# Optimization experiments

Measured on AMD Instinct MI355X. Metric: run time of the kernel, lower is better.

## Reference

```python
import jax, jax.numpy as jnp
import numpy as np

H = 16
D_MODEL = 1024
D_K = D_MODEL // H
B, S = 8, 1024


def setup_inputs() -> dict:
    key = jax.random.key(0)
    ks = jax.random.split(key, 11)
    scale = 1.0 / np.sqrt(D_MODEL)
    inp = {
        "query": jax.random.normal(ks[0], (B, S, D_MODEL), jnp.float32),
        "key_": jax.random.normal(ks[1], (B, S, D_MODEL), jnp.float32),
        "value": jax.random.normal(ks[2], (B, S, D_MODEL), jnp.float32),
        "w_q": jax.random.normal(ks[3], (D_MODEL, D_MODEL), jnp.float32) * scale,
        "b_q": jnp.zeros((D_MODEL,), jnp.float32),
        "w_k": jax.random.normal(ks[4], (D_MODEL, D_MODEL), jnp.float32) * scale,
        "b_k": jnp.zeros((D_MODEL,), jnp.float32),
        "w_v": jax.random.normal(ks[5], (D_MODEL, D_MODEL), jnp.float32) * scale,
        "b_v": jnp.zeros((D_MODEL,), jnp.float32),
        "w_o": jax.random.normal(ks[6], (D_MODEL, D_MODEL), jnp.float32) * scale,
        "b_o": jnp.zeros((D_MODEL,), jnp.float32),
    }
    return inp


def reference(query, key_, value, w_q, b_q, w_k, b_k, w_v, b_v, w_o, b_o):
    # Linear projections (torch Linear: x @ W.T + b), then split heads: [B,S,D] -> [B,H,S,d_k]
    def proj(x, w, b):
        y = jnp.einsum("bsd,ed->bse", x, w) + b
        return y.reshape(B, S, H, D_K).transpose(0, 2, 1, 3)

    q = proj(query, w_q, b_q)
    k = proj(key_, w_k, b_k)
    v = proj(value, w_v, b_v)

    # Scaled dot-product attention (mask=None, dropout p=0 -> identity)
    scores = jnp.einsum("bhqd,bhkd->bhqk", q, k) / jnp.sqrt(jnp.float32(D_K))
    attn = jax.nn.softmax(scores, axis=-1)
    ctx = jnp.einsum("bhqk,bhkd->bhqd", attn, v)  # [B,H,S,d_k]

    # Merge heads and final output projection
    ctx = ctx.transpose(0, 2, 1, 3).reshape(B, S, D_MODEL)
    return jnp.einsum("bsd,ed->bse", ctx, w_o) + b_o
```

## Files before the change

kernel.cpp:

```cpp
#include <hip/hip_runtime.h>
#include <hip/hip_bf16.h>

#define NH 16
#define DK 64
#define BB 8
#define SS 1024
#define DM 1024
#define MTOT (BB * SS)

typedef float f4v __attribute__((ext_vector_type(4)));
typedef short s16v8 __attribute__((ext_vector_type(8)));
typedef unsigned short u16v4 __attribute__((ext_vector_type(4)));
typedef unsigned short u16v8 __attribute__((ext_vector_type(8)));

__device__ __forceinline__ unsigned short f2bf(float x) {
    unsigned int u = __float_as_uint(x);
    u += 0x7FFFu + ((u >> 16) & 1u);
    return (unsigned short)(u >> 16);
}

__device__ __forceinline__ void gload16(const void* g, void* l) {
    __builtin_amdgcn_global_load_lds(
        (const __attribute__((address_space(1))) void*)g,
        (__attribute__((address_space(3))) void*)l, 16, 0, 0);
}

struct Src7 { const float* p[7]; };

__global__ __launch_bounds__(256) void cvt_all(Src7 sp, unsigned short* __restrict__ dst) {
    const size_t e = ((size_t)blockIdx.x * 256 + threadIdx.x) * 8;
    const int unit = (int)(e >> 20);
    int t; size_t base;
    if (unit < 8)       { t = 0; base = 0; }
    else if (unit < 16) { t = 1; base = (size_t)8 << 20; }
    else if (unit < 24) { t = 2; base = (size_t)16 << 20; }
    else                { t = 3 + (unit - 24); base = (size_t)unit << 20; }
    const float* s = sp.p[t] + (e - base);
    f4v a = *(const f4v*)s;
    f4v b = *(const f4v*)(s + 4);
    u16v8 o;
    o[0] = f2bf(a[0]); o[1] = f2bf(a[1]); o[2] = f2bf(a[2]); o[3] = f2bf(a[3]);
    o[4] = f2bf(b[0]); o[5] = f2bf(b[1]); o[6] = f2bf(b[2]); o[7] = f2bf(b[3]);
    *(u16v8*)(dst + e) = o;
}

template <int MODE>
__global__ __launch_bounds__(256) void gemm_bf16(const unsigned short* __restrict__ X,
                                                 const unsigned short* __restrict__ W,
                                                 const float* __restrict__ bias,
                                                 void* __restrict__ Yv) {
    __shared__ unsigned short As[128 * 32];
    __shared__ unsigned short Bs[128 * 32];
    const int tid = threadIdx.x;
    const int wv = tid >> 6, l = tid & 63;
    const int lq = l & 15, g = l >> 4;
    const int wr = wv >> 1, wc = wv & 1;
    const int m0 = blockIdx.y * 128, n0 = blockIdx.x * 128;

    f4v acc[4][4];
#pragma unroll
    for (int i = 0; i < 4; ++i)
#pragma unroll
        for (int j = 0; j < 4; ++j) acc[i][j] = (f4v){0.f, 0.f, 0.f, 0.f};

    for (int kt = 0; kt < DM / 32; ++kt) {
        const int k0 = kt * 32;
        __syncthreads();
#pragma unroll
        for (int p = 0; p < 2; ++p) {
            const int u = p * 256 + tid;
            const int row = u >> 2, kc = u & 3;
            gload16(X + (size_t)(m0 + row) * DM + k0 + kc * 8, As + (size_t)u * 8);
            gload16(W + (size_t)(n0 + row) * DM + k0 + kc * 8, Bs + (size_t)u * 8);
        }
        __syncthreads();

        s16v8 a[4], b[4];
#pragma unroll
        for (int i = 0; i < 4; ++i)
            a[i] = *(const s16v8*)(As + (wr * 64 + i * 16 + lq) * 32 + g * 8);
#pragma unroll
        for (int j = 0; j < 4; ++j)
            b[j] = *(const s16v8*)(Bs + (wc * 64 + j * 16 + lq) * 32 + g * 8);
#pragma unroll
        for (int i = 0; i < 4; ++i)
#pragma unroll
            for (int j = 0; j < 4; ++j)
                acc[i][j] = __builtin_amdgcn_mfma_f32_16x16x32_bf16(a[i], b[j], acc[i][j], 0, 0, 0);
    }

#pragma unroll
    for (int j = 0; j < 4; ++j) {
        const int col = n0 + wc * 64 + j * 16 + lq;
        const float bv = bias[col];
#pragma unroll
        for (int i = 0; i < 4; ++i) {
#pragma unroll
            for (int r = 0; r < 4; ++r) {
                const int row = m0 + wr * 64 + i * 16 + g * 4 + r;
                const float val = acc[i][j][r] + bv;
                if (MODE == 0) {
                    ((float*)Yv)[(size_t)row * DM + col] = val;
                } else {
                    const int b_ = row >> 10, s_ = row & (SS - 1);
                    const int h_ = col >> 6, d_ = col & (DK - 1);
                    ((unsigned short*)Yv)[((size_t)(b_ * NH + h_) * SS + s_) * DK + d_] = f2bf(val);
                }
            }
        }
    }
}

__global__ __launch_bounds__(256) void transpose_v(const unsigned short* __restrict__ Vp,
                                                   unsigned short* __restrict__ VpT) {
    __shared__ unsigned short Ts[64][68];
    const int bx = blockIdx.x;
    const int bh = bx >> 4, kt = bx & 15;
    const unsigned short* src = Vp + (size_t)bh * (SS * DK) + (size_t)kt * 64 * DK;
    unsigned short* dst = VpT + (size_t)bh * (SS * DK) + kt * 64;
    const int t = threadIdx.x;
#pragma unroll
    for (int p = 0; p < 4; ++p) {
        const int idx = p * 1024 + t * 4;
        const int key = idx >> 6, d = idx & 63;
        *(u16v4*)&Ts[key][d] = *(const u16v4*)(src + (size_t)key * DK + d);
    }
    __syncthreads();
#pragma unroll
    for (int p = 0; p < 4; ++p) {
        const int idx = p * 1024 + t * 4;
        const int d = idx >> 6, k4 = idx & 63;
        u16v4 o;
        o[0] = Ts[k4 + 0][d]; o[1] = Ts[k4 + 1][d];
        o[2] = Ts[k4 + 2][d]; o[3] = Ts[k4 + 3][d];
        *(u16v4*)(dst + (size_t)d * SS + k4) = o;
    }
}

__global__ __launch_bounds__(256) void attn_mfma(const unsigned short* __restrict__ Qp,
                                                 const unsigned short* __restrict__ Kp,
                                                 const unsigned short* __restrict__ Vt,
                                                 unsigned short* __restrict__ ctx) {
    __shared__ unsigned short Ks[4096];
    __shared__ unsigned short Vs[4096];
    __shared__ unsigned short Ps[4][16 * 72];
    const int tid = threadIdx.x;
    const int wv = tid >> 6, l = tid & 63;
    const int lq = l & 15, g = l >> 4;
    const int bh = blockIdx.x, q0 = blockIdx.y * 64;

    const unsigned short* Qb = Qp + ((size_t)bh * SS + q0 + wv * 16) * DK;
    const unsigned short* Kb = Kp + (size_t)bh * SS * DK;
    const unsigned short* Vb = Vt + (size_t)bh * DK * SS;

    s16v8 qf[2];
    qf[0] = *(const s16v8*)(Qb + lq * DK + g * 8);
    qf[1] = *(const s16v8*)(Qb + lq * DK + 32 + g * 8);

    f4v O[4];
#pragma unroll
    for (int od = 0; od < 4; ++od) O[od] = (f4v){0.f, 0.f, 0.f, 0.f};
    float m_r[4] = {-1e30f, -1e30f, -1e30f, -1e30f};
    float l_r[4] = {0.f, 0.f, 0.f, 0.f};

    for (int t = 0; t < SS / 64; ++t) {
        __syncthreads();
#pragma unroll
        for (int p = 0; p < 2; ++p) {
            const int u = p * 256 + tid;
            gload16(Kb + (size_t)(t * 64 + (u & 63)) * DK + (u >> 6) * 8, Ks + (size_t)u * 8);
            gload16(Vb + (size_t)(u & 63) * SS + t * 64 + (u >> 6) * 8, Vs + (size_t)u * 8);
        }
        __syncthreads();

        f4v s[4];
#pragma unroll
        for (int ct = 0; ct < 4; ++ct) s[ct] = (f4v){0.f, 0.f, 0.f, 0.f};
#pragma unroll
        for (int kk = 0; kk < 2; ++kk) {
#pragma unroll
            for (int ct = 0; ct < 4; ++ct) {
                s16v8 kf = *(const s16v8*)(Ks + ((kk * 4 + g) * 64 + ct * 16 + lq) * 8);
                s[ct] = __builtin_amdgcn_mfma_f32_16x16x32_bf16(qf[kk], kf, s[ct], 0, 0, 0);
            }
        }

        float rs[4], corr[4];
#pragma unroll
        for (int r = 0; r < 4; ++r) {
            float v = fmaxf(fmaxf(s[0][r], s[1][r]), fmaxf(s[2][r], s[3][r])) * 0.125f;
            v = fmaxf(v, __shfl_xor(v, 1));
            v = fmaxf(v, __shfl_xor(v, 2));
            v = fmaxf(v, __shfl_xor(v, 4));
            v = fmaxf(v, __shfl_xor(v, 8));
            const float mn = fmaxf(m_r[r], v);
            corr[r] = __expf(m_r[r] - mn);
            m_r[r] = mn;
            rs[r] = 0.f;
        }
#pragma unroll
        for (int ct = 0; ct < 4; ++ct) {
#pragma unroll
            for (int r = 0; r < 4; ++r) {
                const float p = __expf(s[ct][r] * 0.125f - m_r[r]);
                rs[r] += p;
                Ps[wv][(g * 4 + r) * 72 + ct * 16 + lq] = f2bf(p);
            }
        }
#pragma unroll
        for (int r = 0; r < 4; ++r) {
            float x = rs[r];
            x += __shfl_xor(x, 1);
            x += __shfl_xor(x, 2);
            x += __shfl_xor(x, 4);
            x += __shfl_xor(x, 8);
            l_r[r] = l_r[r] * corr[r] + x;
        }
#pragma unroll
        for (int od = 0; od < 4; ++od) {
            f4v o = O[od];
            o[0] *= corr[0]; o[1] *= corr[1]; o[2] *= corr[2]; o[3] *= corr[3];
            O[od] = o;
        }

        __builtin_amdgcn_s_waitcnt(0);

#pragma unroll
        for (int kk2 = 0; kk2 < 2; ++kk2) {
            s16v8 pf = *(const s16v8*)(Ps[wv] + lq * 72 + kk2 * 32 + g * 8);
#pragma unroll
            for (int od = 0; od < 4; ++od) {
                s16v8 vf = *(const s16v8*)(Vs + ((kk2 * 4 + g) * 64 + od * 16 + lq) * 8);
                O[od] = __builtin_amdgcn_mfma_f32_16x16x32_bf16(pf, vf, O[od], 0, 0, 0);
            }
        }
    }

    const int b_ = bh >> 4, h_ = bh & 15;
#pragma unroll
    for (int r = 0; r < 4; ++r) {
        const float inv = 1.0f / l_r[r];
        const int sq = q0 + wv * 16 + g * 4 + r;
#pragma unroll
        for (int od = 0; od < 4; ++od) {
            const int d_ = od * 16 + lq;
            ctx[((size_t)b_ * SS + sq) * DM + h_ * DK + d_] = f2bf(O[od][r] * inv);
        }
    }
}

extern "C" void kernel_launch(void* const* d_in, const int* in_sizes, int n_in,
                              void* d_out, int out_size, void* d_ws, size_t ws_size,
                              hipStream_t stream) {
    const float* query = (const float*)d_in[0];
    const float* key_  = (const float*)d_in[1];
    const float* value = (const float*)d_in[2];
    const float* w_q = (const float*)d_in[3];
    const float* b_q = (const float*)d_in[4];
    const float* w_k = (const float*)d_in[5];
    const float* b_k = (const float*)d_in[6];
    const float* w_v = (const float*)d_in[7];
    const float* b_v = (const float*)d_in[8];
    const float* w_o = (const float*)d_in[9];
    const float* b_o = (const float*)d_in[10];

    unsigned short* ws = (unsigned short*)d_ws;
    const size_t NX = (size_t)MTOT * DM;
    const size_t NW = (size_t)DM * DM;
    unsigned short* xq  = ws;
    unsigned short* xk  = xq + NX;
    unsigned short* xv  = xk + NX;
    unsigned short* wqb = xv + NX;
    unsigned short* wkb = wqb + NW;
    unsigned short* wvb = wkb + NW;
    unsigned short* wob = wvb + NW;
    unsigned short* Qp  = wob + NW;
    unsigned short* Kp  = Qp + NX;
    unsigned short* Vp  = Kp + NX;
    unsigned short* VpT = Vp + NX;
    unsigned short* ctx = Vp;

    Src7 sp;
    sp.p[0] = query; sp.p[1] = key_; sp.p[2] = value;
    sp.p[3] = w_q; sp.p[4] = w_k; sp.p[5] = w_v; sp.p[6] = w_o;
    cvt_all<<<14336, 256, 0, stream>>>(sp, ws);

    const dim3 gg(DM / 128, MTOT / 128);
    gemm_bf16<1><<<gg, 256, 0, stream>>>(xq, wqb, b_q, Qp);
    gemm_bf16<1><<<gg, 256, 0, stream>>>(xk, wkb, b_k, Kp);
    gemm_bf16<1><<<gg, 256, 0, stream>>>(xv, wvb, b_v, Vp);

    transpose_v<<<2048, 256, 0, stream>>>(Vp, VpT);

    attn_mfma<<<dim3(BB * NH, SS / 64), 256, 0, stream>>>(Qp, Kp, VpT, ctx);

    gemm_bf16<0><<<gg, 256, 0, stream>>>(ctx, wob, b_o, (float*)d_out);
}
```

Baseline: 388.0 us.

## Batch QKV GEMMs, fuse V transpose, rewrite attention with 32x32 register-resident MFMA

The three QKV projection GEMMs become one launch using blockIdx.z. The V projection writes its output already transposed, so the separate transpose kernel goes away. Attention is rewritten to use 32x32x16 MFMA with K and V loaded straight into registers instead of LDS, with 128 queries per block. Softmax uses exp2 with a prescaled constant and skips the rescale when the max grows by 8 or less, and P is built via lane shuffles rather than an LDS round trip. The trade-offs are higher register pressure, uncoalesced global loads without LDS sharing across waves, and scattered 8-byte stores for the transposed V.

New measurement: 441.0 us. 13.7% more time.

```diff
diff --git a/kernel.cpp b/kernel.cpp
--- a/kernel.cpp
+++ b/kernel.cpp
@@ -9,14 +9,21 @@
 #define MTOT (BB * SS)
 
 typedef float f4v __attribute__((ext_vector_type(4)));
+typedef float f16v __attribute__((ext_vector_type(16)));
 typedef short s16v8 __attribute__((ext_vector_type(8)));
 typedef unsigned short u16v4 __attribute__((ext_vector_type(4)));
 typedef unsigned short u16v8 __attribute__((ext_vector_type(8)));
+
+#define EXP2F(x) __builtin_amdgcn_exp2f(x)
 
 __device__ __forceinline__ unsigned short f2bf(float x) {
     unsigned int u = __float_as_uint(x);
     u += 0x7FFFu + ((u >> 16) & 1u);
     return (unsigned short)(u >> 16);
+}
+
+__device__ __forceinline__ unsigned int packbf2(float lo, float hi) {
+    return ((unsigned int)f2bf(hi) << 16) | f2bf(lo);
 }
 
 __device__ __forceinline__ void gload16(const void* g, void* l) {
@@ -44,11 +51,91 @@
     *(u16v8*)(dst + e) = o;
 }
 
-template <int MODE>
-__global__ __launch_bounds__(256) void gemm_bf16(const unsigned short* __restrict__ X,
-                                                 const unsigned short* __restrict__ W,
-                                                 const float* __restrict__ bias,
-                                                 void* __restrict__ Yv) {
+struct QkvArgs {
+    const unsigned short* X[3];
+    const unsigned short* W[3];
+    const float* bias[3];
+    unsigned short* Y[3];
+};
+
+__global__ __launch_bounds__(256) void gemm_qkv(QkvArgs a) {
+    __shared__ unsigned short As[128 * 32];
+    __shared__ unsigned short Bs[128 * 32];
+    const int z = blockIdx.z;
+    const unsigned short* X = a.X[z];
+    const unsigned short* W = a.W[z];
+    const float* bias = a.bias[z];
+    unsigned short* Y = a.Y[z];
+
+    const int tid = threadIdx.x;
+    const int wv = tid >> 6, l = tid & 63;
+    const int lq = l & 15, g = l >> 4;
+    const int wr = wv >> 1, wc = wv & 1;
+    const int m0 = blockIdx.y * 128, n0 = blockIdx.x * 128;
+
+    f4v acc[4][4];
+#pragma unroll
+    for (int i = 0; i < 4; ++i)
+#pragma unroll
+        for (int j = 0; j < 4; ++j) acc[i][j] = (f4v){0.f, 0.f, 0.f, 0.f};
+
+    for (int kt = 0; kt < DM / 32; ++kt) {
+        const int k0 = kt * 32;
+        __syncthreads();
+#pragma unroll
+        for (int p = 0; p < 2; ++p) {
+            const int u = p * 256 + tid;
+            const int row = u >> 2, kc = u & 3;
+            gload16(X + (size_t)(m0 + row) * DM + k0 + kc * 8, As + (size_t)u * 8);
+            gload16(W + (size_t)(n0 + row) * DM + k0 + kc * 8, Bs + (size_t)u * 8);
+        }
+        __syncthreads();
+
+        s16v8 av[4], bv[4];
+#pragma unroll
+        for (int i = 0; i < 4; ++i)
+            av[i] = *(const s16v8*)(As + (wr * 64 + i * 16 + lq) * 32 + g * 8);
+#pragma unroll
+        for (int j = 0; j < 4; ++j)
+            bv[j] = *(const s16v8*)(Bs + (wc * 64 + j * 16 + lq) * 32 + g * 8);
+#pragma unroll
+        for (int i = 0; i < 4; ++i)
+#pragma unroll
+            for (int j = 0; j < 4; ++j)
+                acc[i][j] = __builtin_amdgcn_mfma_f32_16x16x32_bf16(av[i], bv[j], acc[i][j], 0, 0, 0);
+    }
+
+#pragma unroll
+    for (int j = 0; j < 4; ++j) {
+        const int col = n0 + wc * 64 + j * 16 + lq;
+        const float bvl = bias[col];
+#pragma unroll
+        for (int i = 0; i < 4; ++i) {
+            const int row0 = m0 + wr * 64 + i * 16 + g * 4;
+            if (z < 2) {
+#pragma unroll
+                for (int r = 0; r < 4; ++r) {
+                    const int row = row0 + r;
+                    const int b_ = row >> 10, s_ = row & (SS - 1);
+                    const int h_ = col >> 6, d_ = col & (DK - 1);
+                    Y[((size_t)(b_ * NH + h_) * SS + s_) * DK + d_] = f2bf(acc[i][j][r] + bvl);
+                }
+            } else {
+                const int b_ = row0 >> 10, s0_ = row0 & (SS - 1);
+                const int h_ = col >> 6, d_ = col & (DK - 1);
+                u16v4 o;
+#pragma unroll
+                for (int r = 0; r < 4; ++r) o[r] = f2bf(acc[i][j][r] + bvl);
+                *(u16v4*)&Y[((size_t)(b_ * NH + h_) * DK + d_) * SS + s0_] = o;
+            }
+        }
+    }
+}
+
+__global__ __launch_bounds__(256) void gemm_out(const unsigned short* __restrict__ X,
+                                                const unsigned short* __restrict__ W,
+                                                const float* __restrict__ bias,
+                                                float* __restrict__ Y) {
     __shared__ unsigned short As[128 * 32];
     __shared__ unsigned short Bs[128 * 32];
     const int tid = threadIdx.x;
@@ -75,177 +162,158 @@
         }
         __syncthreads();
 
-        s16v8 a[4], b[4];
+        s16v8 av[4], bv[4];
 #pragma unroll
         for (int i = 0; i < 4; ++i)
-            a[i] = *(const s16v8*)(As + (wr * 64 + i * 16 + lq) * 32 + g * 8);
+            av[i] = *(const s16v8*)(As + (wr * 64 + i * 16 + lq) * 32 + g * 8);
 #pragma unroll
         for (int j = 0; j < 4; ++j)
-            b[j] = *(const s16v8*)(Bs + (wc * 64 + j * 16 + lq) * 32 + g * 8);
+            bv[j] = *(const s16v8*)(Bs + (wc * 64 + j * 16 + lq) * 32 + g * 8);
 #pragma unroll
         for (int i = 0; i < 4; ++i)
 #pragma unroll
             for (int j = 0; j < 4; ++j)
-                acc[i][j] = __builtin_amdgcn_mfma_f32_16x16x32_bf16(a[i], b[j], acc[i][j], 0, 0, 0);
+                acc[i][j] = __builtin_amdgcn_mfma_f32_16x16x32_bf16(av[i], bv[j], acc[i][j], 0, 0, 0);
     }
 
 #pragma unroll
     for (int j = 0; j < 4; ++j) {
         const int col = n0 + wc * 64 + j * 16 + lq;
-        const float bv = bias[col];
+        const float bvl = bias[col];
 #pragma unroll
         for (int i = 0; i < 4; ++i) {
 #pragma unroll
             for (int r = 0; r < 4; ++r) {
                 const int row = m0 + wr * 64 + i * 16 + g * 4 + r;
-                const float val = acc[i][j][r] + bv;
-                if (MODE == 0) {
-                    ((float*)Yv)[(size_t)row * DM + col] = val;
-                } else {
-                    const int b_ = row >> 10, s_ = row & (SS - 1);
-                    const int h_ = col >> 6, d_ = col & (DK - 1);
-                    ((unsigned short*)Yv)[((size_t)(b_ * NH + h_) * SS + s_) * DK + d_] = f2bf(val);
-                }
+                Y[(size_t)row * DM + col] = acc[i][j][r] + bvl;
             }
         }
     }
 }
 
-__global__ __launch_bounds__(256) void transpose_v(const unsigned short* __restrict__ Vp,
-                                                   unsigned short* __restrict__ VpT) {
-    __shared__ unsigned short Ts[64][68];
-    const int bx = blockIdx.x;
-    const int bh = bx >> 4, kt = bx & 15;
-    const unsigned short* src = Vp + (size_t)bh * (SS * DK) + (size_t)kt * 64 * DK;
-    unsigned short* dst = VpT + (size_t)bh * (SS * DK) + kt * 64;
-    const int t = threadIdx.x;
-#pragma unroll
-    for (int p = 0; p < 4; ++p) {
-        const int idx = p * 1024 + t * 4;
-        const int key = idx >> 6, d = idx & 63;
-        *(u16v4*)&Ts[key][d] = *(const u16v4*)(src + (size_t)key * DK + d);
-    }
-    __syncthreads();
-#pragma unroll
-    for (int p = 0; p < 4; ++p) {
-        const int idx = p * 1024 + t * 4;
-        const int d = idx >> 6, k4 = idx & 63;
-        u16v4 o;
-        o[0] = Ts[k4 + 0][d]; o[1] = Ts[k4 + 1][d];
-        o[2] = Ts[k4 + 2][d]; o[3] = Ts[k4 + 3][d];
-        *(u16v4*)(dst + (size_t)d * SS + k4) = o;
-    }
-}
-
-__global__ __launch_bounds__(256) void attn_mfma(const unsigned short* __restrict__ Qp,
-                                                 const unsigned short* __restrict__ Kp,
-                                                 const unsigned short* __restrict__ Vt,
-                                                 unsigned short* __restrict__ ctx) {
-    __shared__ unsigned short Ks[4096];
-    __shared__ unsigned short Vs[4096];
-    __shared__ unsigned short Ps[4][16 * 72];
+__global__ __launch_bounds__(256) void attn_mfma32(const unsigned short* __restrict__ Qp,
+                                                   const unsigned short* __restrict__ Kp,
+                                                   const unsigned short* __restrict__ Vt,
+                                                   unsigned short* __restrict__ ctx) {
     const int tid = threadIdx.x;
-    const int wv = tid >> 6, l = tid & 63;
-    const int lq = l & 15, g = l >> 4;
-    const int bh = blockIdx.x, q0 = blockIdx.y * 64;
-
-    const unsigned short* Qb = Qp + ((size_t)bh * SS + q0 + wv * 16) * DK;
-    const unsigned short* Kb = Kp + (size_t)bh * SS * DK;
-    const unsigned short* Vb = Vt + (size_t)bh * DK * SS;
-
-    s16v8 qf[2];
-    qf[0] = *(const s16v8*)(Qb + lq * DK + g * 8);
-    qf[1] = *(const s16v8*)(Qb + lq * DK + 32 + g * 8);
-
-    f4v O[4];
-#pragma unroll
-    for (int od = 0; od < 4; ++od) O[od] = (f4v){0.f, 0.f, 0.f, 0.f};
-    float m_r[4] = {-1e30f, -1e30f, -1e30f, -1e30f};
-    float l_r[4] = {0.f, 0.f, 0.f, 0.f};
+    const int wv = tid >> 6;
+    const int l = tid & 63;
+    const int l31 = l & 31, hi = l >> 5;
+    const int bh = blockIdx.x;
+    const int q = blockIdx.y * 128 + wv * 32 + l31;
+    const float C = 0.18033688011112042f;
+
+    const unsigned short* Qrow = Qp + ((size_t)bh * SS + q) * DK + hi * 8;
+    s16v8 qf[4];
+#pragma unroll
+    for (int kd = 0; kd < 4; ++kd) qf[kd] = *(const s16v8*)(Qrow + kd * 16);
+
+    const unsigned short* Kb = Kp + (size_t)bh * SS * DK + hi * 8;
+    const unsigned short* Vb = Vt + (size_t)bh * DK * SS + hi * 8;
+
+    f16v O0, O1;
+#pragma unroll
+    for (int r = 0; r < 16; ++r) { O0[r] = 0.f; O1[r] = 0.f; }
+    float me = -1e30f;
+    float lr = 0.f;
 
     for (int t = 0; t < SS / 64; ++t) {
-        __syncthreads();
-#pragma unroll
-        for (int p = 0; p < 2; ++p) {
-            const int u = p * 256 + tid;
-            gload16(Kb + (size_t)(t * 64 + (u & 63)) * DK + (u >> 6) * 8, Ks + (size_t)u * 8);
-            gload16(Vb + (size_t)(u & 63) * SS + t * 64 + (u >> 6) * 8, Vs + (size_t)u * 8);
-        }
-        __syncthreads();
-
-        f4v s[4];
-#pragma unroll
-        for (int ct = 0; ct < 4; ++ct) s[ct] = (f4v){0.f, 0.f, 0.f, 0.f};
-#pragma unroll
-        for (int kk = 0; kk < 2; ++kk) {
-#pragma unroll
-            for (int ct = 0; ct < 4; ++ct) {
-                s16v8 kf = *(const s16v8*)(Ks + ((kk * 4 + g) * 64 + ct * 16 + lq) * 8);
-                s[ct] = __builtin_amdgcn_mfma_f32_16x16x32_bf16(qf[kk], kf, s[ct], 0, 0, 0);
+        s16v8 kf[2][4];
+#pragma unroll
+        for (int ks = 0; ks < 2; ++ks)
+#pragma unroll
+            for (int kd = 0; kd < 4; ++kd)
+                kf[ks][kd] = *(const s16v8*)(Kb + (size_t)(t * 64 + ks * 32 + l31) * DK + kd * 16);
+        s16v8 vf[2][4];
+#pragma unroll
+        for (int db = 0; db < 2; ++db)
+#pragma unroll
+            for (int ksg = 0; ksg < 4; ++ksg)
+                vf[db][ksg] = *(const s16v8*)(Vb + (size_t)(db * 32 + l31) * SS + t * 64 + ksg * 16);
+
+        f16v s0, s1;
+#pragma unroll
+        for (int r = 0; r < 16; ++r) { s0[r] = 0.f; s1[r] = 0.f; }
+#pragma unroll
+        for (int kd = 0; kd < 4; ++kd) {
+            s0 = __builtin_amdgcn_mfma_f32_32x32x16_bf16(kf[0][kd], qf[kd], s0, 0, 0, 0);
+            s1 = __builtin_amdgcn_mfma_f32_32x32x16_bf16(kf[1][kd], qf[kd], s1, 0, 0, 0);
+        }
+
+        float mx = s0[0];
+#pragma unroll
+        for (int r = 1; r < 16; ++r) mx = fmaxf(mx, s0[r]);
+#pragma unroll
+        for (int r = 0; r < 16; ++r) mx = fmaxf(mx, s1[r]);
+        mx = fmaxf(mx, __shfl_xor(mx, 32));
+        const float mxl = mx * C;
+
+        const bool need = !__all(mxl - me <= 8.0f);
+        float corr = 1.0f;
+        if (need) {
+            const float mnew = fmaxf(me, mxl);
+            corr = EXP2F(me - mnew);
+            me = mnew;
+        }
+
+        float rs = 0.f;
+#pragma unroll
+        for (int r = 0; r < 16; ++r) { s0[r] = EXP2F(__fmaf_rn(s0[r], C, -me)); rs += s0[r]; }
+#pragma unroll
+        for (int r = 0; r < 16; ++r) { s1[r] = EXP2F(__fmaf_rn(s1[r], C, -me)); rs += s1[r]; }
+        rs += __shfl_xor(rs, 32);
+        if (need) {
+            lr = lr * corr + rs;
+#pragma unroll
+            for (int r = 0; r < 16; ++r) { O0[r] *= corr; O1[r] *= corr; }
+        } else {
+            lr += rs;
+        }
+
+        s16v8 pb[2][2];
+#pragma unroll
+        for (int ks = 0; ks < 2; ++ks) {
+            unsigned int u[8], su[8];
+#pragma unroll
+            for (int i = 0; i < 8; ++i) {
+                const float plo = (ks == 0) ? s0[2 * i] : s1[2 * i];
+                const float phi = (ks == 0) ? s0[2 * i + 1] : s1[2 * i + 1];
+                u[i] = packbf2(plo, phi);
             }
-        }
-
-        float rs[4], corr[4];
-#pragma unroll
-        for (int r = 0; r < 4; ++r) {
-            float v = fmaxf(fmaxf(s[0][r], s[1][r]), fmaxf(s[2][r], s[3][r])) * 0.125f;
-            v = fmaxf(v, __shfl_xor(v, 1));
-            v = fmaxf(v, __shfl_xor(v, 2));
-            v = fmaxf(v, __shfl_xor(v, 4));
-            v = fmaxf(v, __shfl_xor(v, 8));
-            const float mn = fmaxf(m_r[r], v);
-            corr[r] = __expf(m_r[r] - mn);
-            m_r[r] = mn;
-            rs[r] = 0.f;
-        }
-#pragma unroll
-        for (int ct = 0; ct < 4; ++ct) {
-#pragma unroll
-            for (int r = 0; r < 4; ++r) {
-                const float p = __expf(s[ct][r] * 0.125f - m_r[r]);
-                rs[r] += p;
-                Ps[wv][(g * 4 + r) * 72 + ct * 16 + lq] = f2bf(p);
+#pragma unroll
+            for (int i = 0; i < 8; ++i) su[i] = (unsigned int)__shfl_xor((int)u[i], 32);
+#pragma unroll
+            for (int kk = 0; kk < 2; ++kk) {
+                const int base = 4 * kk + 2 * hi;
+                union { unsigned int w[4]; s16v8 s; } f;
+                f.w[0] = hi ? su[base] : u[base];
+                f.w[1] = hi ? su[base + 1] : u[base + 1];
+                f.w[2] = hi ? u[base] : su[base];
+                f.w[3] = hi ? u[base + 1] : su[base + 1];
+                pb[ks][kk] = f.s;
             }
         }
-#pragma unroll
-        for (int r = 0; r < 4; ++r) {
-            float x = rs[r];
-            x += __shfl_xor(x, 1);
-            x += __shfl_xor(x, 2);
-            x += __shfl_xor(x, 4);
-            x += __shfl_xor(x, 8);
-            l_r[r] = l_r[r] * corr[r] + x;
-        }
-#pragma unroll
-        for (int od = 0; od < 4; ++od) {
-            f4v o = O[od];
-            o[0] *= corr[0]; o[1] *= corr[1]; o[2] *= corr[2]; o[3] *= corr[3];
-            O[od] = o;
-        }
-
-        __builtin_amdgcn_s_waitcnt(0);
-
-#pragma unroll
-        for (int kk2 = 0; kk2 < 2; ++kk2) {
-            s16v8 pf = *(const s16v8*)(Ps[wv] + lq * 72 + kk2 * 32 + g * 8);
-#pragma unroll
-            for (int od = 0; od < 4; ++od) {
-                s16v8 vf = *(const s16v8*)(Vs + ((kk2 * 4 + g) * 64 + od * 16 + lq) * 8);
-                O[od] = __builtin_amdgcn_mfma_f32_16x16x32_bf16(pf, vf, O[od], 0, 0, 0);
-            }
-        }
-    }
-
+
+#pragma unroll
+        for (int ksg = 0; ksg < 4; ++ksg) {
+            O0 = __builtin_amdgcn_mfma_f32_32x32x16_bf16(vf[0][ksg], pb[ksg >> 1][ksg & 1], O0, 0, 0, 0);
+            O1 = __builtin_amdgcn_mfma_f32_32x32x16_bf16(vf[1][ksg], pb[ksg >> 1][ksg & 1], O1, 0, 0, 0);
+        }
+    }
+
+    const float inv = 1.0f / lr;
     const int b_ = bh >> 4, h_ = bh & 15;
-#pragma unroll
-    for (int r = 0; r < 4; ++r) {
-        const float inv = 1.0f / l_r[r];
-        const int sq = q0 + wv * 16 + g * 4 + r;
-#pragma unroll
-        for (int od = 0; od < 4; ++od) {
-            const int d_ = od * 16 + lq;
-            ctx[((size_t)b_ * SS + sq) * DM + h_ * DK + d_] = f2bf(O[od][r] * inv);
-        }
+    unsigned short* crow = ctx + ((size_t)b_ * SS + q) * DM + h_ * DK;
+#pragma unroll
+    for (int g2 = 0; g2 < 4; ++g2) {
+        u16v4 o0, o1;
+#pragma unroll
+        for (int r2 = 0; r2 < 4; ++r2) {
+            o0[r2] = f2bf(O0[4 * g2 + r2] * inv);
+            o1[r2] = f2bf(O1[4 * g2 + r2] * inv);
+        }
+        *(u16v4*)(crow + 8 * g2 + 4 * hi) = o0;
+        *(u16v4*)(crow + 32 + 8 * g2 + 4 * hi) = o1;
     }
 }
 
@@ -276,23 +344,22 @@
     unsigned short* wob = wvb + NW;
     unsigned short* Qp  = wob + NW;
     unsigned short* Kp  = Qp + NX;
-    unsigned short* Vp  = Kp + NX;
-    unsigned short* VpT = Vp + NX;
-    unsigned short* ctx = Vp;
+    unsigned short* VpT = Kp + NX;
+    unsigned short* ctx = xq;
 
     Src7 sp;
     sp.p[0] = query; sp.p[1] = key_; sp.p[2] = value;
     sp.p[3] = w_q; sp.p[4] = w_k; sp.p[5] = w_v; sp.p[6] = w_o;
     cvt_all<<<14336, 256, 0, stream>>>(sp, ws);
 
-    const dim3 gg(DM / 128, MTOT / 128);
-    gemm_bf16<1><<<gg, 256, 0, stream>>>(xq, wqb, b_q, Qp);
-    gemm_bf16<1><<<gg, 256, 0, stream>>>(xk, wkb, b_k, Kp);
-    gemm_bf16<1><<<gg, 256, 0, stream>>>(xv, wvb, b_v, Vp);
-
-    transpose_v<<<2048, 256, 0, stream>>>(Vp, VpT);
-
-    attn_mfma<<<dim3(BB * NH, SS / 64), 256, 0, stream>>>(Qp, Kp, VpT, ctx);
-
-    gemm_bf16<0><<<gg, 256, 0, stream>>>(ctx, wob, b_o, (float*)d_out);
-}
+    QkvArgs qa;
+    qa.X[0] = xq;  qa.X[1] = xk;  qa.X[2] = xv;
+    qa.W[0] = wqb; qa.W[1] = wkb; qa.W[2] = wvb;
+    qa.bias[0] = b_q; qa.bias[1] = b_k; qa.bias[2] = b_v;
+    qa.Y[0] = Qp; qa.Y[1] = Kp; qa.Y[2] = VpT;
+    gemm_qkv<<<dim3(DM / 128, MTOT / 128, 3), 256, 0, stream>>>(qa);
+
+    attn_mfma32<<<dim3(BB * NH, SS / 128), 256, 0, stream>>>(Qp, Kp, VpT, ctx);
+
+    gemm_out<<<dim3(DM / 128, MTOT / 128), 256, 0, stream>>>(ctx, wob, b_o, (float*)d_out);
+}
```
